# Kernel tuning notes

Hardware: AMD Instinct MI355X
Metric: run time of the kernel (lower is better)

Reference implementation:

```python
import jax, jax.numpy as jnp
import numpy as np

E = 1_000_000
NODE_IN = 64
EDGE_IN = 32
GLOBAL_IN = 32
HIDDEN = 128
EDGE_OUT = 32
B = 128


def setup_inputs() -> dict:
    key = jax.random.key(0)
    ks = jax.random.split(key, 10)
    src = jax.random.normal(ks[0], (E, NODE_IN), dtype=jnp.float32)
    dest = jax.random.normal(ks[1], (E, NODE_IN), dtype=jnp.float32)
    edge_attr = jax.random.normal(ks[2], (E, EDGE_IN), dtype=jnp.float32)
    u = jax.random.normal(ks[3], (B, GLOBAL_IN), dtype=jnp.float32)
    edge_batch = jnp.sort(jax.random.randint(ks[4], (E,), 0, B, dtype=jnp.int32)).astype(jnp.int64)
    in_dim = EDGE_IN + 2 * NODE_IN + GLOBAL_IN  # 192
    # Kaiming-uniform-ish init scale, values irrelevant for correctness baseline
    W1 = jax.random.normal(ks[5], (in_dim, HIDDEN), dtype=jnp.float32) * (1.0 / np.sqrt(in_dim))
    b1 = jnp.zeros((HIDDEN,), dtype=jnp.float32)
    W2 = jax.random.normal(ks[6], (HIDDEN, EDGE_OUT), dtype=jnp.float32) * (1.0 / np.sqrt(HIDDEN))
    b2 = jnp.zeros((EDGE_OUT,), dtype=jnp.float32)
    return {"src": src, "dest": dest, "edge_attr": edge_attr, "u": u,
            "edge_batch": edge_batch, "W1": W1, "b1": b1, "W2": W2, "b2": b2}


def reference(src, dest, edge_attr, u, edge_batch, W1, b1, W2, b2):
    # gather per-edge global features: [E, global_in_dim]
    u_expanded = u[edge_batch]
    # concat -> [E, edge_in + 2*node_in + global_in]
    combined = jnp.concatenate([src, dest, edge_attr, u_expanded], axis=1)
    # 2-layer MLP with ReLU
    h = jax.nn.relu(combined @ W1 + b1)
    out = h @ W2 + b2
    return out
```

## Files before the change

### kernel.cpp

```cpp
#include <hip/hip_runtime.h>

#define NODE_IN 64
#define EDGE_IN 32
#define GLOBAL_IN 32
#define HID 128
#define EOUT 32

typedef float f32x4 __attribute__((ext_vector_type(4)));
typedef float f32x2 __attribute__((ext_vector_type(2)));
typedef short s16x8 __attribute__((ext_vector_type(8)));
typedef unsigned short u16x8 __attribute__((ext_vector_type(8)));

#define XROW 384
#define HOFF 24576
#define LDSZ 40960

#define GLOADX4(dst, ptr) asm volatile("global_load_dwordx4 %0, %1, off" : "=v"(dst) : "v"(ptr))
#define GLOADD(dst, ptr)  asm volatile("global_load_dword %0, %1, off"   : "=v"(dst) : "v"(ptr))

__device__ __forceinline__ unsigned short f2bf(float f) {
  __bf16 h = (__bf16)f;
  return __builtin_bit_cast(unsigned short, h);
}

__device__ __forceinline__ s16x8 cvt8(f32x4 a, f32x4 b) {
  u16x8 v = { f2bf(a[0]), f2bf(a[1]), f2bf(a[2]), f2bf(a[3]),
              f2bf(b[0]), f2bf(b[1]), f2bf(b[2]), f2bf(b[3]) };
  return __builtin_bit_cast(s16x8, v);
}

__device__ __forceinline__ void bar_lds() {
  asm volatile("s_waitcnt lgkmcnt(0)" ::: "memory");
  __builtin_amdgcn_s_barrier();
  asm volatile("" ::: "memory");
}

__global__ __launch_bounds__(256) void edge_mlp(
    const float* __restrict__ srcp, const float* __restrict__ dstp,
    const float* __restrict__ eap, const float* __restrict__ up,
    const int* __restrict__ ebp, const float* __restrict__ W1,
    const float* __restrict__ b1, const float* __restrict__ W2,
    const float* __restrict__ b2, float* __restrict__ outp,
    int E, int ntiles)
{
  __shared__ __align__(16) char SM[LDSZ];

  const int t = threadIdx.x;
  const int wid = t >> 6;
  const int lane = t & 63;
  const int g = lane >> 4;
  const int r16 = lane & 15;
  const int rA = t >> 3, cA8 = (t & 7) * 8;
  const int rC = t >> 2, cC8 = (t & 3) * 8;
  const int Em1 = E - 1;

  s16x8 w1f[6][2];
#pragma unroll
  for (int kk = 0; kk < 6; ++kk) {
#pragma unroll
    for (int nt = 0; nt < 2; ++nt) {
      s16x8 v;
#pragma unroll
      for (int j = 0; j < 8; ++j)
        v[j] = (short)f2bf(W1[(32*kk + 8*g + j)*HID + 32*wid + 2*r16 + nt]);
      w1f[kk][nt] = v;
    }
  }
  s16x8 w2f[4][2];
#pragma unroll
  for (int kk = 0; kk < 4; ++kk) {
#pragma unroll
    for (int nt = 0; nt < 2; ++nt) {
      s16x8 v;
#pragma unroll
      for (int j = 0; j < 8; ++j)
        v[j] = (short)f2bf(W2[(32*kk + 8*g + j)*EOUT + 2*r16 + nt]);
      w2f[kk][nt] = v;
    }
  }
  const float b1v0 = b1[32*wid + 2*r16];
  const float b1v1 = b1[32*wid + 2*r16 + 1];
  const float b2v0 = b2[2*r16];
  const float b2v1 = b2[2*r16 + 1];

  f32x4 P0, P1, P2, P3, P4, P5, P6, P7, P8, P9, P10, P11;

  auto issue_gloads = [&](int mb, int eb) {
    const int r0 = min(mb + rA, Em1);
    const int r1 = min(mb + 32 + rA, Em1);
    const int r2 = min(mb + rC, Em1);
    const float* s0 = srcp + (size_t)r0 * NODE_IN + cA8;
    const float* s1 = srcp + (size_t)r1 * NODE_IN + cA8;
    const float* d0 = dstp + (size_t)r0 * NODE_IN + cA8;
    const float* d1 = dstp + (size_t)r1 * NODE_IN + cA8;
    const float* e0 = eap  + (size_t)r2 * EDGE_IN + cC8;
    const float* u0 = up   + (size_t)eb * GLOBAL_IN + cC8;
    GLOADX4(P0, s0);  GLOADX4(P1, s0 + 4);
    GLOADX4(P2, s1);  GLOADX4(P3, s1 + 4);
    GLOADX4(P4, d0);  GLOADX4(P5, d0 + 4);
    GLOADX4(P6, d1);  GLOADX4(P7, d1 + 4);
    GLOADX4(P8, e0);  GLOADX4(P9, e0 + 4);
    GLOADX4(P10, u0); GLOADX4(P11, u0 + 4);
  };

  const int sxw = (t & 7) ^ (rA & 7);
  const int sew = ((t & 3)     ) ^ (rC & 7);
  const int suw = (4 + (t & 3) ) ^ (rC & 7);
  auto write_x = [&]() {
    *(s16x8*)(SM + rA*XROW        + sxw*16)        = cvt8(P0, P1);
    *(s16x8*)(SM + (rA+32)*XROW   + sxw*16)        = cvt8(P2, P3);
    *(s16x8*)(SM + rA*XROW        + (8+sxw)*16)    = cvt8(P4, P5);
    *(s16x8*)(SM + (rA+32)*XROW   + (8+sxw)*16)    = cvt8(P6, P7);
    *(s16x8*)(SM + rC*XROW        + (16+sew)*16)   = cvt8(P8, P9);
    *(s16x8*)(SM + rC*XROW        + (16+suw)*16)   = cvt8(P10, P11);
  };

  int tile = blockIdx.x;
  const int TS = gridDim.x;
  int ebv;

  {
    const int eb0 = ebp[min(tile*64 + rC, Em1)];
    const int eb1 = ebp[min((tile + TS)*64 + rC, Em1)];
    issue_gloads(tile * 64, eb0);
    asm volatile("s_waitcnt vmcnt(0)" ::: "memory");
    __builtin_amdgcn_sched_barrier(0);
    write_x();
    issue_gloads((tile + TS) * 64, eb1);
    GLOADD(ebv, (ebp + min((tile + 2*TS)*64 + rC, Em1)));
  }
  bar_lds();

  for (; tile < ntiles; tile += TS) {
    const int mbase = tile * 64;

    f32x4 acc[4][2];
    {
      const f32x4 z = {0.f, 0.f, 0.f, 0.f};
#pragma unroll
      for (int mi = 0; mi < 4; ++mi) { acc[mi][0] = z; acc[mi][1] = z; }
    }
#pragma unroll
    for (int mi = 0; mi < 4; ++mi) {
      const int r = 16*mi + r16;
      const char* Rp = SM + r * XROW;
      const int s = r16 & 7;
      const s16x8 f0 = *(const s16x8*)(Rp + ((g     ^ s)      )*16);
      const s16x8 f1 = *(const s16x8*)(Rp + (((4+g) ^ s)      )*16);
      const s16x8 f2 = *(const s16x8*)(Rp + ((g     ^ s) +  8 )*16);
      const s16x8 f3 = *(const s16x8*)(Rp + (((4+g) ^ s) +  8 )*16);
      const s16x8 f4 = *(const s16x8*)(Rp + ((g     ^ s) + 16 )*16);
      const s16x8 f5 = *(const s16x8*)(Rp + (((4+g) ^ s) + 16 )*16);
      acc[mi][0] = __builtin_amdgcn_mfma_f32_16x16x32_bf16(f0, w1f[0][0], acc[mi][0], 0, 0, 0);
      acc[mi][1] = __builtin_amdgcn_mfma_f32_16x16x32_bf16(f0, w1f[0][1], acc[mi][1], 0, 0, 0);
      acc[mi][0] = __builtin_amdgcn_mfma_f32_16x16x32_bf16(f1, w1f[1][0], acc[mi][0], 0, 0, 0);
      acc[mi][1] = __builtin_amdgcn_mfma_f32_16x16x32_bf16(f1, w1f[1][1], acc[mi][1], 0, 0, 0);
      acc[mi][0] = __builtin_amdgcn_mfma_f32_16x16x32_bf16(f2, w1f[2][0], acc[mi][0], 0, 0, 0);
      acc[mi][1] = __builtin_amdgcn_mfma_f32_16x16x32_bf16(f2, w1f[2][1], acc[mi][1], 0, 0, 0);
      acc[mi][0] = __builtin_amdgcn_mfma_f32_16x16x32_bf16(f3, w1f[3][0], acc[mi][0], 0, 0, 0);
      acc[mi][1] = __builtin_amdgcn_mfma_f32_16x16x32_bf16(f3, w1f[3][1], acc[mi][1], 0, 0, 0);
      acc[mi][0] = __builtin_amdgcn_mfma_f32_16x16x32_bf16(f4, w1f[4][0], acc[mi][0], 0, 0, 0);
      acc[mi][1] = __builtin_amdgcn_mfma_f32_16x16x32_bf16(f4, w1f[4][1], acc[mi][1], 0, 0, 0);
      acc[mi][0] = __builtin_amdgcn_mfma_f32_16x16x32_bf16(f5, w1f[5][0], acc[mi][0], 0, 0, 0);
      acc[mi][1] = __builtin_amdgcn_mfma_f32_16x16x32_bf16(f5, w1f[5][1], acc[mi][1], 0, 0, 0);
    }

#pragma unroll
    for (int mi = 0; mi < 4; ++mi) {
#pragma unroll
      for (int j = 0; j < 4; ++j) {
        const float h0 = fmaxf(acc[mi][0][j] + b1v0, 0.f);
        const float h1 = fmaxf(acc[mi][1][j] + b1v1, 0.f);
        const unsigned int pk = (unsigned int)f2bf(h0) |
                                ((unsigned int)f2bf(h1) << 16);
        const int row = 16*mi + 4*g + j;
        const int ch = (4*wid + (r16 >> 2)) ^ ((4*g + j) & 7);
        *(unsigned int*)(SM + HOFF + row*256 + ch*16 + (r16 & 3)*4) = pk;
      }
    }
    bar_lds();

    asm volatile("s_waitcnt vmcnt(0)" ::: "memory");
    __builtin_amdgcn_sched_barrier(0);
    write_x();
    issue_gloads((tile + 2*TS) * 64, ebv);
    GLOADD(ebv, (ebp + min((tile + 3*TS)*64 + rC, Em1)));

    f32x4 acc2[2];
    {
      const f32x4 z = {0.f, 0.f, 0.f, 0.f};
      acc2[0] = z; acc2[1] = z;
    }
#pragma unroll
    for (int kk = 0; kk < 4; ++kk) {
      const int ch = (4*kk + g) ^ (r16 & 7);
      const s16x8 ah = *(const s16x8*)(SM + HOFF + (16*wid + r16)*256 + ch*16);
      acc2[0] = __builtin_amdgcn_mfma_f32_16x16x32_bf16(ah, w2f[kk][0], acc2[0], 0, 0, 0);
      acc2[1] = __builtin_amdgcn_mfma_f32_16x16x32_bf16(ah, w2f[kk][1], acc2[1], 0, 0, 0);
    }
#pragma unroll
    for (int j = 0; j < 4; ++j) {
      const int m = mbase + 16*wid + 4*g + j;
      if (m < E) {
        f32x2 o = { acc2[0][j] + b2v0, acc2[1][j] + b2v1 };
        *(f32x2*)(outp + (size_t)m*EOUT + 2*r16) = o;
      }
    }
    bar_lds();
  }
}

extern "C" void kernel_launch(void* const* d_in, const int* in_sizes, int n_in,
                              void* d_out, int out_size, void* d_ws, size_t ws_size,
                              hipStream_t stream) {
  const float* srcp = (const float*)d_in[0];
  const float* dstp = (const float*)d_in[1];
  const float* eap  = (const float*)d_in[2];
  const float* up   = (const float*)d_in[3];
  const int*   ebp  = (const int*)d_in[4];
  const float* W1   = (const float*)d_in[5];
  const float* b1   = (const float*)d_in[6];
  const float* W2   = (const float*)d_in[7];
  const float* b2   = (const float*)d_in[8];
  float* outp = (float*)d_out;

  const int E = in_sizes[0] / NODE_IN;
  const int ntiles = (E + 63) / 64;
  const int grid = ntiles < 2048 ? ntiles : 2048;

  edge_mlp<<<grid, 256, 0, stream>>>(srcp, dstp, eap, up, ebp, W1, b1, W2, b2,
                                     outp, E, ntiles);
}
```

Before: 159.0 us.

## Prepack weights in a prep kernel, stage u in LDS, drop register prefetch

Adds a small prep kernel that converts W1/W2 into bf16 MFMA fragment layout in the workspace, and the main kernel now reads those fragments from global memory on every k-step instead of keeping them resident in registers. The u table is converted once into LDS and gathered per row by edge_batch index, replacing the per-edge u global loads. The asm-based register double-buffered prefetch of the next tile is replaced by synchronous staging at the end of each iteration, and the k-loops are no longer unrolled. This is meant to cut register pressure and redundant u traffic, but it gives up load/compute overlap and adds weight reloads on every tile plus an extra kernel launch.

```diff
diff --git a/kernel.cpp b/kernel.cpp
--- a/kernel.cpp
+++ b/kernel.cpp
@@ -13,10 +13,8 @@
 
 #define XROW 384
 #define HOFF 24576
-#define LDSZ 40960
-
-#define GLOADX4(dst, ptr) asm volatile("global_load_dwordx4 %0, %1, off" : "=v"(dst) : "v"(ptr))
-#define GLOADD(dst, ptr)  asm volatile("global_load_dword %0, %1, off"   : "=v"(dst) : "v"(ptr))
+#define UOFF 40960
+#define LDSZ 49152
 
 __device__ __forceinline__ unsigned short f2bf(float f) {
   __bf16 h = (__bf16)f;
@@ -35,13 +33,32 @@
   asm volatile("" ::: "memory");
 }
 
+__global__ __launch_bounds__(64) void prep_w(const float* __restrict__ W1,
+                                             const float* __restrict__ W2,
+                                             unsigned short* __restrict__ wsf) {
+  const int f = blockIdx.x, l = threadIdx.x;
+  const int lg = l >> 4, lr = l & 15;
+  u16x8 v;
+  if (f < 48) {
+    const int kk = f >> 3, wd = (f >> 1) & 3, nt = f & 1;
+#pragma unroll
+    for (int j = 0; j < 8; ++j)
+      v[j] = f2bf(W1[(32*kk + 8*lg + j)*HID + 32*wd + 2*lr + nt]);
+  } else {
+    const int q = f - 48, kk = q >> 1, nt = q & 1;
+#pragma unroll
+    for (int j = 0; j < 8; ++j)
+      v[j] = f2bf(W2[(32*kk + 8*lg + j)*EOUT + 2*lr + nt]);
+  }
+  *(u16x8*)&wsf[f*512 + l*8] = v;
+}
+
 __global__ __launch_bounds__(256) void edge_mlp(
     const float* __restrict__ srcp, const float* __restrict__ dstp,
     const float* __restrict__ eap, const float* __restrict__ up,
-    const int* __restrict__ ebp, const float* __restrict__ W1,
-    const float* __restrict__ b1, const float* __restrict__ W2,
-    const float* __restrict__ b2, float* __restrict__ outp,
-    int E, int ntiles)
+    const int* __restrict__ ebp, const unsigned short* __restrict__ wsf,
+    const float* __restrict__ b1, const float* __restrict__ b2,
+    float* __restrict__ outp, int E, int ntiles)
 {
   __shared__ __align__(16) char SM[LDSZ];
 
@@ -54,82 +71,60 @@
   const int rC = t >> 2, cC8 = (t & 3) * 8;
   const int Em1 = E - 1;
 
-  s16x8 w1f[6][2];
-#pragma unroll
-  for (int kk = 0; kk < 6; ++kk) {
-#pragma unroll
-    for (int nt = 0; nt < 2; ++nt) {
-      s16x8 v;
-#pragma unroll
-      for (int j = 0; j < 8; ++j)
-        v[j] = (short)f2bf(W1[(32*kk + 8*g + j)*HID + 32*wid + 2*r16 + nt]);
-      w1f[kk][nt] = v;
-    }
-  }
-  s16x8 w2f[4][2];
-#pragma unroll
-  for (int kk = 0; kk < 4; ++kk) {
-#pragma unroll
-    for (int nt = 0; nt < 2; ++nt) {
-      s16x8 v;
-#pragma unroll
-      for (int j = 0; j < 8; ++j)
-        v[j] = (short)f2bf(W2[(32*kk + 8*g + j)*EOUT + 2*r16 + nt]);
-      w2f[kk][nt] = v;
-    }
-  }
   const float b1v0 = b1[32*wid + 2*r16];
   const float b1v1 = b1[32*wid + 2*r16 + 1];
   const float b2v0 = b2[2*r16];
   const float b2v1 = b2[2*r16 + 1];
 
-  f32x4 P0, P1, P2, P3, P4, P5, P6, P7, P8, P9, P10, P11;
-
-  auto issue_gloads = [&](int mb, int eb) {
-    const int r0 = min(mb + rA, Em1);
-    const int r1 = min(mb + 32 + rA, Em1);
-    const int r2 = min(mb + rC, Em1);
+  const int sxw = (t & 7) ^ (rA & 7);
+  const int sew = (t & 3) ^ (rC & 7);
+
+  {
+    const int row = t >> 1, half = t & 1;
+    const float* pu = up + row * GLOBAL_IN + half * 16;
+    const f32x4 u0 = *(const f32x4*)pu,       u1 = *(const f32x4*)(pu + 4);
+    const f32x4 u2 = *(const f32x4*)(pu + 8), u3 = *(const f32x4*)(pu + 12);
+    *(s16x8*)(SM + UOFF + row*64 + half*32)      = cvt8(u0, u1);
+    *(s16x8*)(SM + UOFF + row*64 + half*32 + 16) = cvt8(u2, u3);
+  }
+
+  int bb0, bb1, bb2, bb3;
+  auto load_bb = [&](int tb) {
+    bb0 = ebp[min(tb + r16,      Em1)];
+    bb1 = ebp[min(tb + 16 + r16, Em1)];
+    bb2 = ebp[min(tb + 32 + r16, Em1)];
+    bb3 = ebp[min(tb + 48 + r16, Em1)];
+  };
+
+  auto stage_x = [&](int tb) {
+    const int r0 = min(tb + rA, Em1);
+    const int r1 = min(tb + 32 + rA, Em1);
+    const int r2 = min(tb + rC, Em1);
     const float* s0 = srcp + (size_t)r0 * NODE_IN + cA8;
     const float* s1 = srcp + (size_t)r1 * NODE_IN + cA8;
     const float* d0 = dstp + (size_t)r0 * NODE_IN + cA8;
     const float* d1 = dstp + (size_t)r1 * NODE_IN + cA8;
     const float* e0 = eap  + (size_t)r2 * EDGE_IN + cC8;
-    const float* u0 = up   + (size_t)eb * GLOBAL_IN + cC8;
-    GLOADX4(P0, s0);  GLOADX4(P1, s0 + 4);
-    GLOADX4(P2, s1);  GLOADX4(P3, s1 + 4);
-    GLOADX4(P4, d0);  GLOADX4(P5, d0 + 4);
-    GLOADX4(P6, d1);  GLOADX4(P7, d1 + 4);
-    GLOADX4(P8, e0);  GLOADX4(P9, e0 + 4);
-    GLOADX4(P10, u0); GLOADX4(P11, u0 + 4);
-  };
-
-  const int sxw = (t & 7) ^ (rA & 7);
-  const int sew = ((t & 3)     ) ^ (rC & 7);
-  const int suw = (4 + (t & 3) ) ^ (rC & 7);
-  auto write_x = [&]() {
-    *(s16x8*)(SM + rA*XROW        + sxw*16)        = cvt8(P0, P1);
-    *(s16x8*)(SM + (rA+32)*XROW   + sxw*16)        = cvt8(P2, P3);
-    *(s16x8*)(SM + rA*XROW        + (8+sxw)*16)    = cvt8(P4, P5);
-    *(s16x8*)(SM + (rA+32)*XROW   + (8+sxw)*16)    = cvt8(P6, P7);
-    *(s16x8*)(SM + rC*XROW        + (16+sew)*16)   = cvt8(P8, P9);
-    *(s16x8*)(SM + rC*XROW        + (16+suw)*16)   = cvt8(P10, P11);
+    const f32x4 q0 = *(const f32x4*)s0, q1 = *(const f32x4*)(s0 + 4);
+    const f32x4 q2 = *(const f32x4*)s1, q3 = *(const f32x4*)(s1 + 4);
+    const f32x4 q4 = *(const f32x4*)d0, q5 = *(const f32x4*)(d0 + 4);
+    const f32x4 q6 = *(const f32x4*)d1, q7 = *(const f32x4*)(d1 + 4);
+    const f32x4 q8 = *(const f32x4*)e0, q9 = *(const f32x4*)(e0 + 4);
+    *(s16x8*)(SM + rA*XROW        + sxw*16)     = cvt8(q0, q1);
+    *(s16x8*)(SM + (rA+32)*XROW   + sxw*16)     = cvt8(q2, q3);
+    *(s16x8*)(SM + rA*XROW        + (8+sxw)*16) = cvt8(q4, q5);
+    *(s16x8*)(SM + (rA+32)*XROW   + (8+sxw)*16) = cvt8(q6, q7);
+    *(s16x8*)(SM + rC*XROW        + (16+sew)*16)= cvt8(q8, q9);
   };
 
   int tile = blockIdx.x;
   const int TS = gridDim.x;
-  int ebv;
-
-  {
-    const int eb0 = ebp[min(tile*64 + rC, Em1)];
-    const int eb1 = ebp[min((tile + TS)*64 + rC, Em1)];
-    issue_gloads(tile * 64, eb0);
-    asm volatile("s_waitcnt vmcnt(0)" ::: "memory");
-    __builtin_amdgcn_sched_barrier(0);
-    write_x();
-    issue_gloads((tile + TS) * 64, eb1);
-    GLOADD(ebv, (ebp + min((tile + 2*TS)*64 + rC, Em1)));
-  }
+
+  stage_x(tile * 64);
+  load_bb(tile * 64);
   bar_lds();
+
+  const int s = r16 & 7;
 
   for (; tile < ntiles; tile += TS) {
     const int mbase = tile * 64;
@@ -140,29 +135,32 @@
 #pragma unroll
       for (int mi = 0; mi < 4; ++mi) { acc[mi][0] = z; acc[mi][1] = z; }
     }
-#pragma unroll
-    for (int mi = 0; mi < 4; ++mi) {
-      const int r = 16*mi + r16;
-      const char* Rp = SM + r * XROW;
-      const int s = r16 & 7;
-      const s16x8 f0 = *(const s16x8*)(Rp + ((g     ^ s)      )*16);
-      const s16x8 f1 = *(const s16x8*)(Rp + (((4+g) ^ s)      )*16);
-      const s16x8 f2 = *(const s16x8*)(Rp + ((g     ^ s) +  8 )*16);
-      const s16x8 f3 = *(const s16x8*)(Rp + (((4+g) ^ s) +  8 )*16);
-      const s16x8 f4 = *(const s16x8*)(Rp + ((g     ^ s) + 16 )*16);
-      const s16x8 f5 = *(const s16x8*)(Rp + (((4+g) ^ s) + 16 )*16);
-      acc[mi][0] = __builtin_amdgcn_mfma_f32_16x16x32_bf16(f0, w1f[0][0], acc[mi][0], 0, 0, 0);
-      acc[mi][1] = __builtin_amdgcn_mfma_f32_16x16x32_bf16(f0, w1f[0][1], acc[mi][1], 0, 0, 0);
-      acc[mi][0] = __builtin_amdgcn_mfma_f32_16x16x32_bf16(f1, w1f[1][0], acc[mi][0], 0, 0, 0);
-      acc[mi][1] = __builtin_amdgcn_mfma_f32_16x16x32_bf16(f1, w1f[1][1], acc[mi][1], 0, 0, 0);
-      acc[mi][0] = __builtin_amdgcn_mfma_f32_16x16x32_bf16(f2, w1f[2][0], acc[mi][0], 0, 0, 0);
-      acc[mi][1] = __builtin_amdgcn_mfma_f32_16x16x32_bf16(f2, w1f[2][1], acc[mi][1], 0, 0, 0);
-      acc[mi][0] = __builtin_amdgcn_mfma_f32_16x16x32_bf16(f3, w1f[3][0], acc[mi][0], 0, 0, 0);
-      acc[mi][1] = __builtin_amdgcn_mfma_f32_16x16x32_bf16(f3, w1f[3][1], acc[mi][1], 0, 0, 0);
-      acc[mi][0] = __builtin_amdgcn_mfma_f32_16x16x32_bf16(f4, w1f[4][0], acc[mi][0], 0, 0, 0);
-      acc[mi][1] = __builtin_amdgcn_mfma_f32_16x16x32_bf16(f4, w1f[4][1], acc[mi][1], 0, 0, 0);
-      acc[mi][0] = __builtin_amdgcn_mfma_f32_16x16x32_bf16(f5, w1f[5][0], acc[mi][0], 0, 0, 0);
-      acc[mi][1] = __builtin_amdgcn_mfma_f32_16x16x32_bf16(f5, w1f[5][1], acc[mi][1], 0, 0, 0);
+#pragma unroll 1
+    for (int kk = 0; kk < 6; ++kk) {
+      const s16x8 w0 = *(const s16x8*)&wsf[(kk*8 + wid*2 + 0)*512 + lane*8];
+      const s16x8 w1 = *(const s16x8*)&wsf[(kk*8 + wid*2 + 1)*512 + lane*8];
+      s16x8 f0, f1, f2, f3;
+      if (kk == 5) {
+        f0 = *(const s16x8*)(SM + UOFF + bb0*64 + g*16);
+        f1 = *(const s16x8*)(SM + UOFF + bb1*64 + g*16);
+        f2 = *(const s16x8*)(SM + UOFF + bb2*64 + g*16);
+        f3 = *(const s16x8*)(SM + UOFF + bb3*64 + g*16);
+      } else {
+        const int phys = ((kk >> 1) << 3) + ((4*(kk & 1) + g) ^ s);
+        const char* base = SM + phys*16;
+        f0 = *(const s16x8*)(base + (r16     )*XROW);
+        f1 = *(const s16x8*)(base + (16 + r16)*XROW);
+        f2 = *(const s16x8*)(base + (32 + r16)*XROW);
+        f3 = *(const s16x8*)(base + (48 + r16)*XROW);
+      }
+      acc[0][0] = __builtin_amdgcn_mfma_f32_16x16x32_bf16(f0, w0, acc[0][0], 0, 0, 0);
+      acc[0][1] = __builtin_amdgcn_mfma_f32_16x16x32_bf16(f0, w1, acc[0][1], 0, 0, 0);
+      acc[1][0] = __builtin_amdgcn_mfma_f32_16x16x32_bf16(f1, w0, acc[1][0], 0, 0, 0);
+      acc[1][1] = __builtin_amdgcn_mfma_f32_16x16x32_bf16(f1, w1, acc[1][1], 0, 0, 0);
+      acc[2][0] = __builtin_amdgcn_mfma_f32_16x16x32_bf16(f2, w0, acc[2][0], 0, 0, 0);
+      acc[2][1] = __builtin_amdgcn_mfma_f32_16x16x32_bf16(f2, w1, acc[2][1], 0, 0, 0);
+      acc[3][0] = __builtin_amdgcn_mfma_f32_16x16x32_bf16(f3, w0, acc[3][0], 0, 0, 0);
+      acc[3][1] = __builtin_amdgcn_mfma_f32_16x16x32_bf16(f3, w1, acc[3][1], 0, 0, 0);
     }
 
 #pragma unroll
@@ -180,32 +178,28 @@
     }
     bar_lds();
 
-    asm volatile("s_waitcnt vmcnt(0)" ::: "memory");
-    __builtin_amdgcn_sched_barrier(0);
-    write_x();
-    issue_gloads((tile + 2*TS) * 64, ebv);
-    GLOADD(ebv, (ebp + min((tile + 3*TS)*64 + rC, Em1)));
-
-    f32x4 acc2[2];
-    {
-      const f32x4 z = {0.f, 0.f, 0.f, 0.f};
-      acc2[0] = z; acc2[1] = z;
-    }
-#pragma unroll
-    for (int kk = 0; kk < 4; ++kk) {
-      const int ch = (4*kk + g) ^ (r16 & 7);
+    f32x4 a20, a21;
+    { const f32x4 z = {0.f, 0.f, 0.f, 0.f}; a20 = z; a21 = z; }
+#pragma unroll 1
+    for (int kk2 = 0; kk2 < 4; ++kk2) {
+      const s16x8 v0 = *(const s16x8*)&wsf[(48 + kk2*2 + 0)*512 + lane*8];
+      const s16x8 v1 = *(const s16x8*)&wsf[(48 + kk2*2 + 1)*512 + lane*8];
+      const int ch = (4*kk2 + g) ^ s;
       const s16x8 ah = *(const s16x8*)(SM + HOFF + (16*wid + r16)*256 + ch*16);
-      acc2[0] = __builtin_amdgcn_mfma_f32_16x16x32_bf16(ah, w2f[kk][0], acc2[0], 0, 0, 0);
-      acc2[1] = __builtin_amdgcn_mfma_f32_16x16x32_bf16(ah, w2f[kk][1], acc2[1], 0, 0, 0);
+      a20 = __builtin_amdgcn_mfma_f32_16x16x32_bf16(ah, v0, a20, 0, 0, 0);
+      a21 = __builtin_amdgcn_mfma_f32_16x16x32_bf16(ah, v1, a21, 0, 0, 0);
     }
 #pragma unroll
     for (int j = 0; j < 4; ++j) {
       const int m = mbase + 16*wid + 4*g + j;
       if (m < E) {
-        f32x2 o = { acc2[0][j] + b2v0, acc2[1][j] + b2v1 };
+        f32x2 o = { a20[j] + b2v0, a21[j] + b2v1 };
         *(f32x2*)(outp + (size_t)m*EOUT + 2*r16) = o;
       }
     }
+
+    stage_x((tile + TS) * 64);
+    load_bb((tile + TS) * 64);
     bar_lds();
   }
 }
@@ -223,11 +217,13 @@
   const float* W2   = (const float*)d_in[7];
   const float* b2   = (const float*)d_in[8];
   float* outp = (float*)d_out;
+  unsigned short* wsf = (unsigned short*)d_ws;
 
   const int E = in_sizes[0] / NODE_IN;
   const int ntiles = (E + 63) / 64;
   const int grid = ntiles < 2048 ? ntiles : 2048;
 
-  edge_mlp<<<grid, 256, 0, stream>>>(srcp, dstp, eap, up, ebp, W1, b1, W2, b2,
+  prep_w<<<56, 64, 0, stream>>>(W1, W2, wsf);
+  edge_mlp<<<grid, 256, 0, stream>>>(srcp, dstp, eap, up, ebp, wsf, b1, b2,
                                      outp, E, ntiles);
 }
```

New measurement: 177.4 us. 1.12x slower.
